# Kernel tuning notes

Measured on AMD Instinct MI355X. Metric: run time of the kernel, lower is better.

Reference implementation:

```python
import jax, jax.numpy as jnp
import numpy as np

H = 1024
EPS = 1e-5
N_ENT = 1000
TOP_K = 5


def _ln(x, g, b):
    mu = jnp.mean(x, axis=-1, keepdims=True)
    var = jnp.mean((x - mu) ** 2, axis=-1, keepdims=True)
    return (x - mu) * jax.lax.rsqrt(var + EPS) * g + b


def _gelu(x):
    return jax.nn.gelu(x, approximate=False)  # torch nn.GELU default (erf)


def setup_inputs() -> dict:
    key = jax.random.key(0)
    ks = jax.random.split(key, 24)
    s = 0.02
    inp = {
        'hidden_states': jax.random.normal(ks[0], (8, 2048, H), jnp.float32),
        'entity_embeddings': jax.random.normal(ks[1], (N_ENT, H), jnp.float32) * 0.01,
        # entity_encoder: H -> 2H -> H -> LN
        'ee_w1': jax.random.normal(ks[2], (H, 2 * H), jnp.float32) * s,
        'ee_b1': jnp.zeros((2 * H,), jnp.float32),
        'ee_w2': jax.random.normal(ks[3], (2 * H, H), jnp.float32) * s,
        'ee_b2': jnp.zeros((H,), jnp.float32),
        'ee_g': jnp.ones((H,), jnp.float32),
        'ee_beta': jnp.zeros((H,), jnp.float32),
        # relation_encoder: H -> H -> H -> LN
        're_w1': jax.random.normal(ks[4], (H, H), jnp.float32) * s,
        're_b1': jnp.zeros((H,), jnp.float32),
        're_w2': jax.random.normal(ks[5], (H, H), jnp.float32) * s,
        're_b2': jnp.zeros((H,), jnp.float32),
        're_g': jnp.ones((H,), jnp.float32),
        're_beta': jnp.zeros((H,), jnp.float32),
        # reasoning_network: 3H -> 2H -> H -> LN
        'rn_w1': jax.random.normal(ks[6], (3 * H, 2 * H), jnp.float32) * s,
        'rn_b1': jnp.zeros((2 * H,), jnp.float32),
        'rn_w2': jax.random.normal(ks[7], (2 * H, H), jnp.float32) * s,
        'rn_b2': jnp.zeros((H,), jnp.float32),
        'rn_g': jnp.ones((H,), jnp.float32),
        'rn_beta': jnp.zeros((H,), jnp.float32),
        # validation_network: H -> H/2 -> 1 -> sigmoid
        'vn_w1': jax.random.normal(ks[8], (H, H // 2), jnp.float32) * s,
        'vn_b1': jnp.zeros((H // 2,), jnp.float32),
        'vn_w2': jax.random.normal(ks[9], (H // 2, 1), jnp.float32) * s,
        'vn_b2': jnp.zeros((1,), jnp.float32),
    }
    return inp


def reference(hidden_states, entity_embeddings,
              ee_w1, ee_b1, ee_w2, ee_b2, ee_g, ee_beta,
              re_w1, re_b1, re_w2, re_b2, re_g, re_beta,
              rn_w1, rn_b1, rn_w2, rn_b2, rn_g, rn_beta,
              vn_w1, vn_b1, vn_w2, vn_b2):
    # entity encoder over all tokens: [B,S,H]
    entity_features = _ln(_gelu(hidden_states @ ee_w1 + ee_b1) @ ee_w2 + ee_b2, ee_g, ee_beta)

    # query=None path: relation encoder on mean-pooled hidden states [B,H]
    pooled = jnp.mean(hidden_states, axis=1)
    relation_features = _ln(_gelu(pooled @ re_w1 + re_b1) @ re_w2 + re_b2, re_g, re_beta)
    query_features = relation_features

    # similarity + top-k entity retrieval
    entity_similarities = query_features @ entity_embeddings.T  # [B, N_ENT]
    top_values, top_indices = jax.lax.top_k(entity_similarities, TOP_K)
    retrieved_entities = entity_embeddings[top_indices]  # [B, K, H]

    # reasoning input: [mean retrieved entity | relation | mean context]
    entity_vec = jnp.mean(retrieved_entities, axis=1)  # [B,H]
    context_vec = jnp.mean(hidden_states, axis=1)      # [B,H]
    reasoning_in = jnp.concatenate([entity_vec, relation_features, context_vec], axis=-1)  # [B,3H]
    reasoning_output = _ln(_gelu(reasoning_in @ rn_w1 + rn_b1) @ rn_w2 + rn_b2, rn_g, rn_beta)

    validation_scores = jax.nn.sigmoid(_gelu(reasoning_output @ vn_w1 + vn_b1) @ vn_w2 + vn_b2)

    return (entity_features, relation_features, retrieved_entities,
            entity_similarities, top_indices, reasoning_output, validation_scores)
```

## Files before the change

kernel.cpp:

```cpp
#include <hip/hip_runtime.h>
#include <math.h>

#define H 1024
#define SEQ 2048
#define BATCH 8
#define N_ENT 1000
#define TOPK 5
#define LN_EPS 1e-5f

using bf16x8 = __attribute__((ext_vector_type(8))) __bf16;
using f32x4  = __attribute__((ext_vector_type(4))) float;
#define AS1 __attribute__((address_space(1)))
#define AS3 __attribute__((address_space(3)))


__device__ __forceinline__ float gelu_fast(float x) {
    float z = fabsf(x) * 0.70710678118654752440f;
    float t = __builtin_amdgcn_rcpf(fmaf(0.3275911f, z, 1.0f));
    float p = fmaf(fmaf(fmaf(fmaf(1.061405429f, t, -1.453152027f), t, 1.421413741f),
                        t, -0.284496736f), t, 0.254829592f) * t;
    float e = __builtin_amdgcn_exp2f(-z * z * 1.44269504088896f);
    float erfz = fmaf(-p, e, 1.0f);
    float s = copysignf(erfz, x);
    return 0.5f * x * (1.0f + s);
}

__device__ __forceinline__ float sigmoidf_(float x) {
    return 1.0f / (1.0f + expf(-x));
}

__device__ __forceinline__ unsigned short f2bf(float f) {
    unsigned int u = __float_as_uint(f);
    unsigned int r = (u + 0x7fffu + ((u >> 16) & 1u)) >> 16;
    return (unsigned short)r;
}

__device__ float block_sum(float v, float* red) {
    for (int off = 32; off > 0; off >>= 1) v += __shfl_down(v, off, 64);
    int wid = threadIdx.x >> 6;
    int lane = threadIdx.x & 63;
    int nw = blockDim.x >> 6;
    if (lane == 0) red[wid] = v;
    __syncthreads();
    if (threadIdx.x == 0) {
        float s = 0.f;
        for (int i = 0; i < nw; ++i) s += red[i];
        red[0] = s;
    }
    __syncthreads();
    float r = red[0];
    __syncthreads();
    return r;
}


__global__ void f2bf_kernel(const float* __restrict__ in, unsigned short* __restrict__ out, int n) {
    int i = (blockIdx.x * blockDim.x + threadIdx.x) * 4;
    if (i >= n) return;
    float4 v = *(const float4*)(in + i);
    ushort4 o;
    o.x = f2bf(v.x); o.y = f2bf(v.y); o.z = f2bf(v.z); o.w = f2bf(v.w);
    *(ushort4*)(out + i) = o;
}

__global__ void transpose_bf_kernel(const float* __restrict__ in, unsigned short* __restrict__ out,
                                    int R, int C) {
    __shared__ float tile[32][33];
    int c0 = blockIdx.x * 32, r0 = blockIdx.y * 32;
    int tx = threadIdx.x & 31, ty = threadIdx.x >> 5;
#pragma unroll
    for (int i = 0; i < 32; i += 8)
        tile[ty + i][tx] = in[(size_t)(r0 + ty + i) * C + c0 + tx];
    __syncthreads();
#pragma unroll
    for (int i = 0; i < 32; i += 8)
        out[(size_t)(c0 + ty + i) * R + r0 + tx] = f2bf(tile[tx][ty + i]);
}


__global__ void pool1_kernel(const float* __restrict__ hs, float* __restrict__ part,
                             unsigned short* __restrict__ hsb) {
    int sc = blockIdx.x, b = blockIdx.y, t = threadIdx.x;
    size_t rowbase = (size_t)b * SEQ + sc * 64;
    const float* p = hs + rowbase * H + t * 4;
    float4 a = {0.f, 0.f, 0.f, 0.f};
    for (int s = 0; s < 64; ++s) {
        float4 v = *(const float4*)(p + (size_t)s * H);
        a.x += v.x; a.y += v.y; a.z += v.z; a.w += v.w;
        if (hsb) {
            ushort4 o;
            o.x = f2bf(v.x); o.y = f2bf(v.y); o.z = f2bf(v.z); o.w = f2bf(v.w);
            *(ushort4*)(hsb + (rowbase + s) * H + t * 4) = o;
        }
    }
    *(float4*)(part + ((size_t)b * 32 + sc) * H + t * 4) = a;
}

__global__ void pool2_kernel(const float* __restrict__ part, float* __restrict__ pooled) {
    int b = blockIdx.x, t = threadIdx.x;
    float4 s = {0.f, 0.f, 0.f, 0.f};
    for (int sc = 0; sc < 32; ++sc) {
        float4 v = *(const float4*)(part + ((size_t)b * 32 + sc) * H + t * 4);
        s.x += v.x; s.y += v.y; s.z += v.z; s.w += v.w;
    }
    float4 o = {s.x * (1.0f / SEQ), s.y * (1.0f / SEQ), s.z * (1.0f / SEQ), s.w * (1.0f / SEQ)};
    *(float4*)(pooled + (size_t)b * H + t * 4) = o;
}


template <int KRANGE>
__global__ void mlp_partial_kernel(const float* __restrict__ X, int ldx,
                                   const float* __restrict__ W, int N,
                                   float* __restrict__ part) {
    __shared__ float xs[8][KRANGE];
    int jb = blockIdx.x, ks = blockIdx.y, t = threadIdx.x;
    int k0 = ks * KRANGE;
    for (int i = t; i < 8 * KRANGE; i += 256) {
        int b = i / KRANGE, k = i % KRANGE;
        xs[b][k] = X[(size_t)b * ldx + k0 + k];
    }
    __syncthreads();
    int j = jb * 256 + t;
    float acc[8] = {};
    for (int k = 0; k < KRANGE; ++k) {
        float w = W[(size_t)(k0 + k) * N + j];
#pragma unroll
        for (int b = 0; b < 8; ++b) acc[b] = fmaf(xs[b][k], w, acc[b]);
    }
#pragma unroll
    for (int b = 0; b < 8; ++b) part[((size_t)ks * 8 + b) * N + j] = acc[b];
}

__global__ void mlp_reduce_gelu_kernel(const float* __restrict__ part, const float* __restrict__ bias,
                                       float* __restrict__ out, int N, int nks) {
    int b = blockIdx.y;
    int j = blockIdx.x * 256 + threadIdx.x;
    float s = bias[j];
    for (int ks = 0; ks < nks; ++ks) s += part[((size_t)ks * 8 + b) * N + j];
    out[(size_t)b * N + j] = gelu_fast(s);
}

__global__ void mlp_reduce_ln_kernel(const float* __restrict__ part, const float* __restrict__ bias,
                                     const float* __restrict__ g, const float* __restrict__ be,
                                     float* __restrict__ out, int nks) {
    __shared__ float red[32];
    int b = blockIdx.x, t = threadIdx.x;
    float s = bias[t];
    for (int ks = 0; ks < nks; ++ks) s += part[((size_t)ks * 8 + b) * H + t];
    float mu = block_sum(s, red) * (1.0f / H);
    float d = s - mu;
    float var = block_sum(d * d, red) * (1.0f / H);
    out[(size_t)b * H + t] = d * rsqrtf(var + LN_EPS) * g[t] + be[t];
}


__global__ void sim_kernel(const float* __restrict__ rel, const float* __restrict__ ent,
                           float* __restrict__ sims) {
    __shared__ float rl[8 * H];
    int t = threadIdx.x;
    for (int i = t; i < 8 * H; i += 256) rl[i] = rel[i];
    __syncthreads();
    int e = blockIdx.x * 4 + (t >> 6);
    int lane = t & 63;
    float ev[16];
    const float* ep = ent + (size_t)e * H;
#pragma unroll
    for (int i = 0; i < 16; ++i) ev[i] = ep[lane + i * 64];
#pragma unroll
    for (int b = 0; b < 8; ++b) {
        float a = 0.f;
#pragma unroll
        for (int i = 0; i < 16; ++i) a = fmaf(ev[i], rl[b * H + lane + i * 64], a);
        for (int off = 32; off > 0; off >>= 1) a += __shfl_down(a, off, 64);
        if (lane == 0) sims[b * N_ENT + e] = a;
    }
}

__global__ void topk_kernel(const float* __restrict__ sims, float* __restrict__ out_idx_f,
                            int* __restrict__ idx_i) {
    __shared__ float v[1024];
    __shared__ float rv[4];
    __shared__ int ri[4];
    int b = blockIdx.x, t = threadIdx.x;
    for (int i = t; i < 1024; i += 256) v[i] = (i < N_ENT) ? sims[b * N_ENT + i] : -INFINITY;
    __syncthreads();
    for (int k = 0; k < TOPK; ++k) {
        float best = -INFINITY;
        int bi = 0x7fffffff;
        for (int i = t; i < 1024; i += 256) {
            float x = v[i];
            if (x > best || (x == best && i < bi)) { best = x; bi = i; }
        }
        for (int off = 32; off > 0; off >>= 1) {
            float ov = __shfl_down(best, off, 64);
            int oi = __shfl_down(bi, off, 64);
            if (ov > best || (ov == best && oi < bi)) { best = ov; bi = oi; }
        }
        if ((t & 63) == 0) { rv[t >> 6] = best; ri[t >> 6] = bi; }
        __syncthreads();
        if (t == 0) {
            for (int w = 1; w < 4; ++w)
                if (rv[w] > rv[0] || (rv[w] == rv[0] && ri[w] < ri[0])) { rv[0] = rv[w]; ri[0] = ri[w]; }
            int sel = ri[0];
            out_idx_f[b * TOPK + k] = (float)sel;
            idx_i[b * TOPK + k] = sel;
            v[sel] = -INFINITY;
        }
        __syncthreads();
    }
}

__global__ void gather_concat_kernel(const float* __restrict__ ent, const int* __restrict__ idx,
                                     const float* __restrict__ rel, const float* __restrict__ pooled,
                                     float* __restrict__ retrieved, float* __restrict__ xin) {
    int b = blockIdx.x, h = threadIdx.x;
    float acc = 0.f;
    for (int k = 0; k < TOPK; ++k) {
        float v = ent[(size_t)idx[b * TOPK + k] * H + h];
        retrieved[((size_t)b * TOPK + k) * H + h] = v;
        acc += v;
    }
    float* xb = xin + (size_t)b * 3 * H;
    xb[h] = acc * (1.0f / TOPK);
    xb[H + h] = rel[b * H + h];
    xb[2 * H + h] = pooled[b * H + h];
}

__global__ void vn_final_kernel(const float* __restrict__ part, const float* __restrict__ b1,
                                const float* __restrict__ w2, const float* __restrict__ b2,
                                float* __restrict__ vs, int nks) {
    __shared__ float red[32];
    int b = blockIdx.x, t = threadIdx.x;
    float s = b1[t];
    for (int ks = 0; ks < nks; ++ks) s += part[((size_t)ks * 8 + b) * 512 + t];
    float c = gelu_fast(s) * w2[t];
    float tot = block_sum(c, red);
    if (t == 0) vs[b] = sigmoidf_(tot + b2[0]);
}

template <int GELU_BF16_OUT>
__global__ __launch_bounds__(512, 2) void gemm256_8ph(const unsigned short* __restrict__ A,
                                                      const unsigned short* __restrict__ Bt,
                                                      const float* __restrict__ bias,
                                                      void* __restrict__ Cout,
                                                      int M, int N, int K) {
    __shared__ __align__(16) unsigned short As[4][128 * 64];
    __shared__ __align__(16) unsigned short Bs[4][128 * 64];
    const int tid = threadIdx.x;
    const int lane = tid & 63;
    const int w = tid >> 6;
    const int wm2 = w >> 2;
    const int wn4 = w & 3;

    const int Np = N >> 8;
    const int nwg = gridDim.x;
    int bid = blockIdx.x;
    int s = bid;
    if ((nwg & 7) == 0) s = (bid & 7) * (nwg >> 3) + (bid >> 3);
    const int m0 = (s / Np) << 8;
    const int n0 = (s % Np) << 8;

    const int nT = K >> 6;

    const int l7 = lane & 7;
    const int lrow0 = w * 16 + (lane >> 3);
    const int lrow1 = lrow0 + 8;
    const int kel0 = ((l7 ^ (lrow0 & 7)) << 3);
    const int kel1 = ((l7 ^ (lrow1 & 7)) << 3);
    const unsigned short* pa0 = A + (size_t)(m0 + lrow0) * K + kel0;
    const unsigned short* pa1 = A + (size_t)(m0 + lrow1) * K + kel1;
    const unsigned short* pb0 = Bt + (size_t)(n0 + lrow0) * K + kel0;
    const unsigned short* pb1 = Bt + (size_t)(n0 + lrow1) * K + kel1;
    const size_t halfstep = (size_t)128 * K;
    const int dst0 = (w * 16) * 64;
    const int dst1 = dst0 + 8 * 64;

    auto stageA = [&](int t, int half) {
        if (t >= nT) return;
        int slot = (2 * t + half) & 3;
        int koff = t << 6;
        __builtin_amdgcn_global_load_lds((AS1 void*)(pa0 + half * halfstep + koff),
                                         (AS3 void*)(&As[slot][dst0]), 16, 0, 0);
        __builtin_amdgcn_global_load_lds((AS1 void*)(pa1 + half * halfstep + koff),
                                         (AS3 void*)(&As[slot][dst1]), 16, 0, 0);
    };
    auto stageB = [&](int t, int half) {
        if (t >= nT) return;
        int slot = (2 * t + half) & 3;
        int koff = t << 6;
        __builtin_amdgcn_global_load_lds((AS1 void*)(pb0 + half * halfstep + koff),
                                         (AS3 void*)(&Bs[slot][dst0]), 16, 0, 0);
        __builtin_amdgcn_global_load_lds((AS1 void*)(pb1 + half * halfstep + koff),
                                         (AS3 void*)(&Bs[slot][dst1]), 16, 0, 0);
    };

    const int arow = lane & 15;
    const int xk0 = (((lane >> 4) << 4)) ^ (l7 << 4);
    const int xk1 = (64 + ((lane >> 4) << 4)) ^ (l7 << 4);
    auto ldf = [&](const unsigned short* slotbase, int rowbase, int xk) -> bf16x8 {
        return *(const bf16x8*)((const char*)slotbase + (rowbase + arow) * 128 + xk);
    };

    f32x4 acc[8][4] = {};

    stageA(0, 0); stageA(0, 1); stageB(0, 0); stageB(0, 1);
    asm volatile("s_waitcnt vmcnt(4)" ::: "memory");
    stageA(1, 0); stageB(1, 0); stageB(1, 1);
    asm volatile("s_waitcnt vmcnt(6)" ::: "memory");
    __builtin_amdgcn_s_barrier();

    bf16x8 af0[4][2], af1[4][2], bf0[2][2], bf1[2][2];

    for (int T = 0; T < nT; ++T) {
        const unsigned short* Aslot0 = As[(2 * T) & 3];
        const unsigned short* Aslot1 = As[(2 * T + 1) & 3];
        const unsigned short* Bslot0 = Bs[(2 * T) & 3];
        const unsigned short* Bslot1 = Bs[(2 * T + 1) & 3];

#pragma unroll
        for (int ii = 0; ii < 4; ++ii) {
            af0[ii][0] = ldf(Aslot0, ii * 32 + wm2 * 16, xk0);
            af0[ii][1] = ldf(Aslot0, ii * 32 + wm2 * 16, xk1);
        }
#pragma unroll
        for (int jj = 0; jj < 2; ++jj) {
            bf0[jj][0] = ldf(Bslot0, jj * 64 + wn4 * 16, xk0);
            bf0[jj][1] = ldf(Bslot0, jj * 64 + wn4 * 16, xk1);
        }
        stageA(T + 1, 1);
        __builtin_amdgcn_s_barrier();
        __builtin_amdgcn_s_setprio(1);
#pragma unroll
        for (int ii = 0; ii < 4; ++ii)
#pragma unroll
            for (int jj = 0; jj < 2; ++jj) {
                acc[ii][jj] = __builtin_amdgcn_mfma_f32_16x16x32_bf16(af0[ii][0], bf0[jj][0], acc[ii][jj], 0, 0, 0);
                acc[ii][jj] = __builtin_amdgcn_mfma_f32_16x16x32_bf16(af0[ii][1], bf0[jj][1], acc[ii][jj], 0, 0, 0);
            }
        __builtin_amdgcn_s_setprio(0);
        __builtin_amdgcn_s_barrier();

#pragma unroll
        for (int jj = 0; jj < 2; ++jj) {
            bf1[jj][0] = ldf(Bslot1, jj * 64 + wn4 * 16, xk0);
            bf1[jj][1] = ldf(Bslot1, jj * 64 + wn4 * 16, xk1);
        }
        stageA(T + 2, 0);
        __builtin_amdgcn_s_barrier();
        __builtin_amdgcn_s_setprio(1);
#pragma unroll
        for (int ii = 0; ii < 4; ++ii)
#pragma unroll
            for (int jj = 0; jj < 2; ++jj) {
                acc[ii][2 + jj] = __builtin_amdgcn_mfma_f32_16x16x32_bf16(af0[ii][0], bf1[jj][0], acc[ii][2 + jj], 0, 0, 0);
                acc[ii][2 + jj] = __builtin_amdgcn_mfma_f32_16x16x32_bf16(af0[ii][1], bf1[jj][1], acc[ii][2 + jj], 0, 0, 0);
            }
        __builtin_amdgcn_s_setprio(0);
        __builtin_amdgcn_s_barrier();

#pragma unroll
        for (int ii = 0; ii < 4; ++ii) {
            af1[ii][0] = ldf(Aslot1, ii * 32 + wm2 * 16, xk0);
            af1[ii][1] = ldf(Aslot1, ii * 32 + wm2 * 16, xk1);
        }
        stageB(T + 2, 0);
        __builtin_amdgcn_s_barrier();
        __builtin_amdgcn_s_setprio(1);
#pragma unroll
        for (int ii = 0; ii < 4; ++ii)
#pragma unroll
            for (int jj = 0; jj < 2; ++jj) {
                acc[4 + ii][jj] = __builtin_amdgcn_mfma_f32_16x16x32_bf16(af1[ii][0], bf0[jj][0], acc[4 + ii][jj], 0, 0, 0);
                acc[4 + ii][jj] = __builtin_amdgcn_mfma_f32_16x16x32_bf16(af1[ii][1], bf0[jj][1], acc[4 + ii][jj], 0, 0, 0);
            }
        __builtin_amdgcn_s_setprio(0);
        __builtin_amdgcn_s_barrier();

        stageB(T + 2, 1);
        if (T + 3 <= nT) {
            asm volatile("s_waitcnt vmcnt(6)" ::: "memory");
        } else {
            asm volatile("s_waitcnt vmcnt(0)" ::: "memory");
        }
        __builtin_amdgcn_s_barrier();
        __builtin_amdgcn_s_setprio(1);
#pragma unroll
        for (int ii = 0; ii < 4; ++ii)
#pragma unroll
            for (int jj = 0; jj < 2; ++jj) {
                acc[4 + ii][2 + jj] = __builtin_amdgcn_mfma_f32_16x16x32_bf16(af1[ii][0], bf1[jj][0], acc[4 + ii][2 + jj], 0, 0, 0);
                acc[4 + ii][2 + jj] = __builtin_amdgcn_mfma_f32_16x16x32_bf16(af1[ii][1], bf1[jj][1], acc[4 + ii][2 + jj], 0, 0, 0);
            }
        __builtin_amdgcn_s_setprio(0);
        __builtin_amdgcn_s_barrier();
    }

    const int cn = lane & 15;
    const int rbase = (lane >> 4) * 4;
#pragma unroll
    for (int i = 0; i < 8; ++i) {
        int mbase = m0 + (i >> 2) * 128 + (i & 3) * 32 + wm2 * 16 + rbase;
#pragma unroll
        for (int j = 0; j < 4; ++j) {
            int n = n0 + (j >> 1) * 128 + (j & 1) * 64 + wn4 * 16 + cn;
            float bv = bias[n];
#pragma unroll
            for (int r = 0; r < 4; ++r) {
                float c = acc[i][j][r] + bv;
                if (GELU_BF16_OUT) {
                    c = gelu_fast(c);
                    ((unsigned short*)Cout)[(size_t)(mbase + r) * N + n] = f2bf(c);
                } else {
                    ((float*)Cout)[(size_t)(mbase + r) * N + n] = c;
                }
            }
        }
    }
}

__global__ void ln_rows_kernel(float* __restrict__ x, const float* __restrict__ g,
                               const float* __restrict__ beta) {
    __shared__ float red[32];
    float* p = x + (size_t)blockIdx.x * H;
    int t = threadIdx.x;
    float4 v = *(const float4*)(p + t * 4);
    float s = v.x + v.y + v.z + v.w;
    float mu = block_sum(s, red) * (1.0f / H);
    float4 d = { v.x - mu, v.y - mu, v.z - mu, v.w - mu };
    float d2 = d.x * d.x + d.y * d.y + d.z * d.z + d.w * d.w;
    float var = block_sum(d2, red) * (1.0f / H);
    float inv = rsqrtf(var + LN_EPS);
    float4 gg = *(const float4*)(g + t * 4);
    float4 bb = *(const float4*)(beta + t * 4);
    float4 o = { d.x * inv * gg.x + bb.x, d.y * inv * gg.y + bb.y,
                 d.z * inv * gg.z + bb.z, d.w * inv * gg.w + bb.w };
    *(float4*)(p + t * 4) = o;
}


extern "C" void kernel_launch(void* const* d_in, const int* in_sizes, int n_in,
                              void* d_out, int out_size, void* d_ws, size_t ws_size,
                              hipStream_t stream) {
    const float* hs     = (const float*)d_in[0];
    const float* ent    = (const float*)d_in[1];
    const float* ee_w1  = (const float*)d_in[2];
    const float* ee_b1  = (const float*)d_in[3];
    const float* ee_w2  = (const float*)d_in[4];
    const float* ee_b2  = (const float*)d_in[5];
    const float* ee_g   = (const float*)d_in[6];
    const float* ee_be  = (const float*)d_in[7];
    const float* re_w1  = (const float*)d_in[8];
    const float* re_b1  = (const float*)d_in[9];
    const float* re_w2  = (const float*)d_in[10];
    const float* re_b2  = (const float*)d_in[11];
    const float* re_g   = (const float*)d_in[12];
    const float* re_be  = (const float*)d_in[13];
    const float* rn_w1  = (const float*)d_in[14];
    const float* rn_b1  = (const float*)d_in[15];
    const float* rn_w2  = (const float*)d_in[16];
    const float* rn_b2  = (const float*)d_in[17];
    const float* rn_g   = (const float*)d_in[18];
    const float* rn_be  = (const float*)d_in[19];
    const float* vn_w1  = (const float*)d_in[20];
    const float* vn_b1  = (const float*)d_in[21];
    const float* vn_w2  = (const float*)d_in[22];
    const float* vn_b2  = (const float*)d_in[23];

    float* out = (float*)d_out;
    float* ef   = out;
    float* rel  = ef + (size_t)BATCH * SEQ * H;
    float* retr = rel + BATCH * H;
    float* sims = retr + BATCH * TOPK * H;
    float* tidx = sims + BATCH * N_ENT;
    float* ro   = tidx + BATCH * TOPK;
    float* vs   = ro + BATCH * H;

    float* ws = (float*)d_ws;
    size_t o = 0;
    float* pooled = ws + o; o += 8192;
    int*   idx_i  = (int*)(ws + o); o += 64;
    float* xin    = ws + o; o += 8 * 3 * H;
    float* h1r    = ws + o; o += 8 * H;
    float* h1n    = ws + o; o += 8 * 2 * H;
    float* part   = ws + o; o += 24 * 8 * 2048;
    unsigned short* w1t = (unsigned short*)(ws + o); o += (2048 * 1024) / 2;
    unsigned short* w2t = (unsigned short*)(ws + o); o += (2048 * 1024) / 2;
    unsigned short* hsb = (unsigned short*)(ws + o);

    long long avail = (long long)(ws_size / 4) - (long long)o;
    int chunk = (int)(avail / 1536);
    chunk &= ~255;
    int total = BATCH * SEQ;
    if (chunk > total) chunk = total;
    if (chunk < 256) chunk = 256;
    bool full = (chunk >= total);
    unsigned short* midb = hsb + (size_t)chunk * H;

    transpose_bf_kernel<<<dim3(2048 / 32, 1024 / 32), 256, 0, stream>>>(ee_w1, w1t, 1024, 2048);
    transpose_bf_kernel<<<dim3(1024 / 32, 2048 / 32), 256, 0, stream>>>(ee_w2, w2t, 2048, 1024);

    pool1_kernel<<<dim3(32, BATCH), 256, 0, stream>>>(hs, part, full ? hsb : nullptr);
    pool2_kernel<<<BATCH, 256, 0, stream>>>(part, pooled);

    mlp_partial_kernel<64><<<dim3(4, 16), 256, 0, stream>>>(pooled, H, re_w1, H, part);
    mlp_reduce_gelu_kernel<<<dim3(4, 8), 256, 0, stream>>>(part, re_b1, h1r, H, 16);
    mlp_partial_kernel<64><<<dim3(4, 16), 256, 0, stream>>>(h1r, H, re_w2, H, part);
    mlp_reduce_ln_kernel<<<BATCH, 1024, 0, stream>>>(part, re_b2, re_g, re_be, rel, 16);

    sim_kernel<<<250, 256, 0, stream>>>(rel, ent, sims);
    topk_kernel<<<BATCH, 256, 0, stream>>>(sims, tidx, idx_i);
    gather_concat_kernel<<<BATCH, 1024, 0, stream>>>(ent, idx_i, rel, pooled, retr, xin);

    mlp_partial_kernel<128><<<dim3(8, 24), 256, 0, stream>>>(xin, 3 * H, rn_w1, 2 * H, part);
    mlp_reduce_gelu_kernel<<<dim3(8, 8), 256, 0, stream>>>(part, rn_b1, h1n, 2 * H, 24);
    mlp_partial_kernel<128><<<dim3(4, 16), 256, 0, stream>>>(h1n, 2 * H, rn_w2, H, part);
    mlp_reduce_ln_kernel<<<BATCH, 1024, 0, stream>>>(part, rn_b2, rn_g, rn_be, ro, 16);

    mlp_partial_kernel<128><<<dim3(2, 8), 256, 0, stream>>>(ro, H, vn_w1, 512, part);
    vn_final_kernel<<<BATCH, 512, 0, stream>>>(part, vn_b1, vn_w2, vn_b2, vs, 8);

    for (int r0 = 0; r0 < total; r0 += chunk) {
        int m = total - r0;
        if (m > chunk) m = chunk;
        if (!full) {
            int nconv = m * H;
            f2bf_kernel<<<(nconv / 4 + 255) / 256, 256, 0, stream>>>(hs + (size_t)r0 * H, hsb, nconv);
        }
        unsigned short* a1 = full ? (hsb + (size_t)r0 * H) : hsb;
        gemm256_8ph<1><<<(m / 256) * (2048 / 256), 512, 0, stream>>>(a1, w1t, ee_b1, midb,
                                                                     m, 2048, 1024);
        gemm256_8ph<0><<<(m / 256) * (1024 / 256), 512, 0, stream>>>(midb, w2t, ee_b2,
                                                                     ef + (size_t)r0 * H,
                                                                     m, 1024, 2048);
    }
    ln_rows_kernel<<<total, 256, 0, stream>>>(ef, ee_g, ee_be);
}
```

Before: 537.1 us.

## Fuse small-path kernels into one persistent kernel with grid barriers

Replaces the chain of about fourteen small launches (pool reduce, relation MLP, similarity, top-k, gather, reasoning MLP, validation) with a single 64-block persistent kernel that uses an atomic global barrier between stages. The two weight transposes are also merged into one launch. The goal is to cut per-launch overhead and idle gaps on the small serial path. The cost is that 64 blocks give little parallelism for the weight-streaming MLP stages, and the spin barrier relies on all 64 blocks being co-resident.

```diff
diff --git a/kernel.cpp b/kernel.cpp
--- a/kernel.cpp
+++ b/kernel.cpp
@@ -7,6 +7,7 @@
 #define N_ENT 1000
 #define TOPK 5
 #define LN_EPS 1e-5f
+#define NB_SMALL 64
 
 using bf16x8 = __attribute__((ext_vector_type(8))) __bf16;
 using f32x4  = __attribute__((ext_vector_type(4))) float;
@@ -53,6 +54,24 @@
     return r;
 }
 
+__device__ __forceinline__ void gbar(unsigned* cnt, unsigned* gen) {
+    __syncthreads();
+    if (threadIdx.x == 0) {
+        __threadfence();
+        unsigned g = __hip_atomic_load(gen, __ATOMIC_RELAXED, __HIP_MEMORY_SCOPE_AGENT);
+        unsigned a = __hip_atomic_fetch_add(cnt, 1u, __ATOMIC_ACQ_REL, __HIP_MEMORY_SCOPE_AGENT);
+        if (a == NB_SMALL - 1) {
+            __hip_atomic_store(cnt, 0u, __ATOMIC_RELAXED, __HIP_MEMORY_SCOPE_AGENT);
+            __hip_atomic_fetch_add(gen, 1u, __ATOMIC_ACQ_REL, __HIP_MEMORY_SCOPE_AGENT);
+        } else {
+            while (__hip_atomic_load(gen, __ATOMIC_ACQUIRE, __HIP_MEMORY_SCOPE_AGENT) == g)
+                __builtin_amdgcn_s_sleep(1);
+        }
+        __threadfence();
+    }
+    __syncthreads();
+}
+
 
 __global__ void f2bf_kernel(const float* __restrict__ in, unsigned short* __restrict__ out, int n) {
     int i = (blockIdx.x * blockDim.x + threadIdx.x) * 4;
@@ -63,10 +82,14 @@
     *(ushort4*)(out + i) = o;
 }
 
-__global__ void transpose_bf_kernel(const float* __restrict__ in, unsigned short* __restrict__ out,
-                                    int R, int C) {
+__global__ void transpose_both_kernel(const float* __restrict__ w1, unsigned short* __restrict__ o1,
+                                      const float* __restrict__ w2, unsigned short* __restrict__ o2) {
     __shared__ float tile[32][33];
-    int c0 = blockIdx.x * 32, r0 = blockIdx.y * 32;
+    int bid = blockIdx.x;
+    const float* in; unsigned short* out; int R, C, bx, by;
+    if (bid < 2048) { in = w1; out = o1; R = 1024; C = 2048; bx = bid & 63; by = bid >> 6; }
+    else { bid -= 2048; in = w2; out = o2; R = 2048; C = 1024; bx = bid & 31; by = bid >> 5; }
+    int c0 = bx * 32, r0 = by * 32;
     int tx = threadIdx.x & 31, ty = threadIdx.x >> 5;
 #pragma unroll
     for (int i = 0; i < 32; i += 8)
@@ -96,146 +119,211 @@
     *(float4*)(part + ((size_t)b * 32 + sc) * H + t * 4) = a;
 }
 
-__global__ void pool2_kernel(const float* __restrict__ part, float* __restrict__ pooled) {
-    int b = blockIdx.x, t = threadIdx.x;
-    float4 s = {0.f, 0.f, 0.f, 0.f};
-    for (int sc = 0; sc < 32; ++sc) {
-        float4 v = *(const float4*)(part + ((size_t)b * 32 + sc) * H + t * 4);
-        s.x += v.x; s.y += v.y; s.z += v.z; s.w += v.w;
-    }
-    float4 o = {s.x * (1.0f / SEQ), s.y * (1.0f / SEQ), s.z * (1.0f / SEQ), s.w * (1.0f / SEQ)};
-    *(float4*)(pooled + (size_t)b * H + t * 4) = o;
-}
-
-
-template <int KRANGE>
-__global__ void mlp_partial_kernel(const float* __restrict__ X, int ldx,
-                                   const float* __restrict__ W, int N,
-                                   float* __restrict__ part) {
-    __shared__ float xs[8][KRANGE];
-    int jb = blockIdx.x, ks = blockIdx.y, t = threadIdx.x;
-    int k0 = ks * KRANGE;
-    for (int i = t; i < 8 * KRANGE; i += 256) {
-        int b = i / KRANGE, k = i % KRANGE;
-        xs[b][k] = X[(size_t)b * ldx + k0 + k];
+
+__device__ void mlp_partial_dev(const float* X, int ldx, const float* W, int N,
+                                float* part, int jb, int ks, int KR, float* xs) {
+    int t = threadIdx.x;
+    int k0 = ks * KR;
+    __syncthreads();
+    for (int i = t; i < 8 * KR; i += 256) {
+        int b = i / KR, k = i - b * KR;
+        xs[b * KR + k] = X[(size_t)b * ldx + k0 + k];
     }
     __syncthreads();
     int j = jb * 256 + t;
     float acc[8] = {};
-    for (int k = 0; k < KRANGE; ++k) {
+    for (int k = 0; k < KR; ++k) {
         float w = W[(size_t)(k0 + k) * N + j];
 #pragma unroll
-        for (int b = 0; b < 8; ++b) acc[b] = fmaf(xs[b][k], w, acc[b]);
-    }
-#pragma unroll
-    for (int b = 0; b < 8; ++b) part[((size_t)ks * 8 + b) * N + j] = acc[b];
-}
-
-__global__ void mlp_reduce_gelu_kernel(const float* __restrict__ part, const float* __restrict__ bias,
-                                       float* __restrict__ out, int N, int nks) {
-    int b = blockIdx.y;
-    int j = blockIdx.x * 256 + threadIdx.x;
-    float s = bias[j];
-    for (int ks = 0; ks < nks; ++ks) s += part[((size_t)ks * 8 + b) * N + j];
-    out[(size_t)b * N + j] = gelu_fast(s);
-}
-
-__global__ void mlp_reduce_ln_kernel(const float* __restrict__ part, const float* __restrict__ bias,
-                                     const float* __restrict__ g, const float* __restrict__ be,
-                                     float* __restrict__ out, int nks) {
-    __shared__ float red[32];
-    int b = blockIdx.x, t = threadIdx.x;
-    float s = bias[t];
-    for (int ks = 0; ks < nks; ++ks) s += part[((size_t)ks * 8 + b) * H + t];
-    float mu = block_sum(s, red) * (1.0f / H);
-    float d = s - mu;
-    float var = block_sum(d * d, red) * (1.0f / H);
-    out[(size_t)b * H + t] = d * rsqrtf(var + LN_EPS) * g[t] + be[t];
-}
-
-
-__global__ void sim_kernel(const float* __restrict__ rel, const float* __restrict__ ent,
-                           float* __restrict__ sims) {
-    __shared__ float rl[8 * H];
+        for (int b = 0; b < 8; ++b) acc[b] = fmaf(xs[b * KR + k], w, acc[b]);
+    }
+#pragma unroll
+    for (int b = 0; b < 8; ++b) part[((size_t)(ks * 8 + b)) * N + j] = acc[b];
+}
+
+__device__ void reduce_ln_256(const float* part, const float* bias, const float* g,
+                              const float* be, float* out, int nks, int b, float* red) {
     int t = threadIdx.x;
-    for (int i = t; i < 8 * H; i += 256) rl[i] = rel[i];
-    __syncthreads();
-    int e = blockIdx.x * 4 + (t >> 6);
-    int lane = t & 63;
-    float ev[16];
-    const float* ep = ent + (size_t)e * H;
-#pragma unroll
-    for (int i = 0; i < 16; ++i) ev[i] = ep[lane + i * 64];
-#pragma unroll
-    for (int b = 0; b < 8; ++b) {
-        float a = 0.f;
-#pragma unroll
-        for (int i = 0; i < 16; ++i) a = fmaf(ev[i], rl[b * H + lane + i * 64], a);
-        for (int off = 32; off > 0; off >>= 1) a += __shfl_down(a, off, 64);
-        if (lane == 0) sims[b * N_ENT + e] = a;
-    }
-}
-
-__global__ void topk_kernel(const float* __restrict__ sims, float* __restrict__ out_idx_f,
-                            int* __restrict__ idx_i) {
-    __shared__ float v[1024];
-    __shared__ float rv[4];
-    __shared__ int ri[4];
-    int b = blockIdx.x, t = threadIdx.x;
-    for (int i = t; i < 1024; i += 256) v[i] = (i < N_ENT) ? sims[b * N_ENT + i] : -INFINITY;
-    __syncthreads();
-    for (int k = 0; k < TOPK; ++k) {
-        float best = -INFINITY;
-        int bi = 0x7fffffff;
-        for (int i = t; i < 1024; i += 256) {
-            float x = v[i];
-            if (x > best || (x == best && i < bi)) { best = x; bi = i; }
-        }
-        for (int off = 32; off > 0; off >>= 1) {
-            float ov = __shfl_down(best, off, 64);
-            int oi = __shfl_down(bi, off, 64);
-            if (ov > best || (ov == best && oi < bi)) { best = ov; bi = oi; }
-        }
-        if ((t & 63) == 0) { rv[t >> 6] = best; ri[t >> 6] = bi; }
+    float4 s = *(const float4*)(bias + t * 4);
+    for (int ks = 0; ks < nks; ++ks) {
+        float4 p = *(const float4*)(part + (((size_t)(ks * 8 + b)) << 10) + t * 4);
+        s.x += p.x; s.y += p.y; s.z += p.z; s.w += p.w;
+    }
+    float mu = block_sum(s.x + s.y + s.z + s.w, red) * (1.0f / H);
+    float4 d = {s.x - mu, s.y - mu, s.z - mu, s.w - mu};
+    float var = block_sum(d.x * d.x + d.y * d.y + d.z * d.z + d.w * d.w, red) * (1.0f / H);
+    float inv = rsqrtf(var + LN_EPS);
+    float4 gg = *(const float4*)(g + t * 4);
+    float4 bb = *(const float4*)(be + t * 4);
+    float4 o = {d.x * inv * gg.x + bb.x, d.y * inv * gg.y + bb.y,
+                d.z * inv * gg.z + bb.z, d.w * inv * gg.w + bb.w};
+    *(float4*)(out + ((size_t)b << 10) + t * 4) = o;
+}
+
+__global__ __launch_bounds__(256) void small_path_kernel(
+    float* part,
+    float* pooled, float* h1r, float* h1n, float* xin, int* idx_i,
+    const float* __restrict__ ent,
+    const float* re_w1, const float* re_b1, const float* re_w2, const float* re_b2,
+    const float* re_g, const float* re_be,
+    const float* rn_w1, const float* rn_b1, const float* rn_w2, const float* rn_b2,
+    const float* rn_g, const float* rn_be,
+    const float* vn_w1, const float* vn_b1, const float* vn_w2, const float* vn_b2,
+    float* rel, float* sims, float* tidx, float* retr, float* ro, float* vs,
+    unsigned* bar) {
+    __shared__ __align__(16) unsigned char smraw[33 * 1024];
+    float* xs  = (float*)smraw;
+    float* rl  = (float*)smraw;
+    float* tkv = (float*)smraw;
+    float* trv = (float*)(smraw + 4096);
+    int*   tri = (int*)(smraw + 4112);
+    float* red = (float*)smraw;
+
+    unsigned* cnt = bar;
+    unsigned* gen = bar + 1;
+    const int bid = blockIdx.x;
+    const int t = threadIdx.x;
+
+    {
+        int gid = bid * 256 + t;
+        if (gid < 8 * H) {
+            int b = gid >> 10, h = gid & 1023;
+            float s = 0.f;
+            for (int sc = 0; sc < 32; ++sc) s += part[(((size_t)(b * 32 + sc)) << 10) + h];
+            pooled[((size_t)b << 10) + h] = s * (1.0f / SEQ);
+        }
+    }
+    gbar(cnt, gen);
+
+    mlp_partial_dev(pooled, H, re_w1, H, part, bid & 3, bid >> 2, 64, xs);
+    gbar(cnt, gen);
+
+    if (bid < 32) {
+        int jb = bid & 3, b = bid >> 2;
+        int j = jb * 256 + t;
+        float s = re_b1[j];
+        for (int ks = 0; ks < 16; ++ks) s += part[((size_t)(ks * 8 + b)) * H + j];
+        h1r[((size_t)b << 10) + j] = gelu_fast(s);
+    }
+    gbar(cnt, gen);
+
+    mlp_partial_dev(h1r, H, re_w2, H, part, bid & 3, bid >> 2, 64, xs);
+    gbar(cnt, gen);
+
+    if (bid < 8) reduce_ln_256(part, re_b2, re_g, re_be, rel, 16, bid, red);
+    gbar(cnt, gen);
+
+    {
+        for (int i = t; i < 8 * H; i += 256) rl[i] = rel[i];
         __syncthreads();
-        if (t == 0) {
-            for (int w = 1; w < 4; ++w)
-                if (rv[w] > rv[0] || (rv[w] == rv[0] && ri[w] < ri[0])) { rv[0] = rv[w]; ri[0] = ri[w]; }
-            int sel = ri[0];
-            out_idx_f[b * TOPK + k] = (float)sel;
-            idx_i[b * TOPK + k] = sel;
-            v[sel] = -INFINITY;
-        }
+        int widx = t >> 6, lane = t & 63;
+        for (int r = 0; r < 4; ++r) {
+            int e = bid * 16 + r * 4 + widx;
+            if (e < N_ENT) {
+                const float* ep = ent + (size_t)e * H;
+                float ev[16];
+#pragma unroll
+                for (int i = 0; i < 16; ++i) ev[i] = ep[lane + i * 64];
+#pragma unroll
+                for (int b = 0; b < 8; ++b) {
+                    float a = 0.f;
+#pragma unroll
+                    for (int i = 0; i < 16; ++i) a = fmaf(ev[i], rl[b * H + lane + i * 64], a);
+                    for (int off = 32; off > 0; off >>= 1) a += __shfl_down(a, off, 64);
+                    if (lane == 0) sims[b * N_ENT + e] = a;
+                }
+            }
+        }
+    }
+    gbar(cnt, gen);
+
+    if (bid < 8) {
+        int b = bid;
+        for (int i = t; i < 1024; i += 256) tkv[i] = (i < N_ENT) ? sims[b * N_ENT + i] : -INFINITY;
         __syncthreads();
-    }
-}
-
-__global__ void gather_concat_kernel(const float* __restrict__ ent, const int* __restrict__ idx,
-                                     const float* __restrict__ rel, const float* __restrict__ pooled,
-                                     float* __restrict__ retrieved, float* __restrict__ xin) {
-    int b = blockIdx.x, h = threadIdx.x;
-    float acc = 0.f;
-    for (int k = 0; k < TOPK; ++k) {
-        float v = ent[(size_t)idx[b * TOPK + k] * H + h];
-        retrieved[((size_t)b * TOPK + k) * H + h] = v;
-        acc += v;
-    }
-    float* xb = xin + (size_t)b * 3 * H;
-    xb[h] = acc * (1.0f / TOPK);
-    xb[H + h] = rel[b * H + h];
-    xb[2 * H + h] = pooled[b * H + h];
-}
-
-__global__ void vn_final_kernel(const float* __restrict__ part, const float* __restrict__ b1,
-                                const float* __restrict__ w2, const float* __restrict__ b2,
-                                float* __restrict__ vs, int nks) {
-    __shared__ float red[32];
-    int b = blockIdx.x, t = threadIdx.x;
-    float s = b1[t];
-    for (int ks = 0; ks < nks; ++ks) s += part[((size_t)ks * 8 + b) * 512 + t];
-    float c = gelu_fast(s) * w2[t];
-    float tot = block_sum(c, red);
-    if (t == 0) vs[b] = sigmoidf_(tot + b2[0]);
+        for (int k = 0; k < TOPK; ++k) {
+            float best = -INFINITY;
+            int bi = 0x7fffffff;
+            for (int i = t; i < 1024; i += 256) {
+                float x = tkv[i];
+                if (x > best || (x == best && i < bi)) { best = x; bi = i; }
+            }
+            for (int off = 32; off > 0; off >>= 1) {
+                float ov = __shfl_down(best, off, 64);
+                int oi = __shfl_down(bi, off, 64);
+                if (ov > best || (ov == best && oi < bi)) { best = ov; bi = oi; }
+            }
+            if ((t & 63) == 0) { trv[t >> 6] = best; tri[t >> 6] = bi; }
+            __syncthreads();
+            if (t == 0) {
+                for (int w = 1; w < 4; ++w)
+                    if (trv[w] > trv[0] || (trv[w] == trv[0] && tri[w] < tri[0])) { trv[0] = trv[w]; tri[0] = tri[w]; }
+                int sel = tri[0];
+                tidx[b * TOPK + k] = (float)sel;
+                idx_i[b * TOPK + k] = sel;
+                tkv[sel] = -INFINITY;
+            }
+            __syncthreads();
+        }
+    }
+    gbar(cnt, gen);
+
+    if (bid < 8) {
+        int b = bid;
+#pragma unroll
+        for (int u = 0; u < 4; ++u) {
+            int h = u * 256 + t;
+            float acc = 0.f;
+            for (int k = 0; k < TOPK; ++k) {
+                float v = ent[(size_t)idx_i[b * TOPK + k] * H + h];
+                retr[((size_t)(b * TOPK + k)) * H + h] = v;
+                acc += v;
+            }
+            xin[(size_t)b * 3 * H + h] = acc * (1.0f / TOPK);
+            xin[(size_t)b * 3 * H + H + h] = rel[b * H + h];
+            xin[(size_t)b * 3 * H + 2 * H + h] = pooled[b * H + h];
+        }
+    }
+    gbar(cnt, gen);
+
+    for (int r = 0; r < 3; ++r) {
+        int u = bid + 64 * r;
+        mlp_partial_dev(xin, 3 * H, rn_w1, 2 * H, part, u & 7, u >> 3, 128, xs);
+    }
+    gbar(cnt, gen);
+
+    {
+        int jb = bid & 7, b = bid >> 3;
+        int j = jb * 256 + t;
+        float s = rn_b1[j];
+        for (int ks = 0; ks < 24; ++ks) s += part[((size_t)(ks * 8 + b)) * 2048 + j];
+        h1n[(size_t)b * 2048 + j] = gelu_fast(s);
+    }
+    gbar(cnt, gen);
+
+    mlp_partial_dev(h1n, 2 * H, rn_w2, H, part, bid & 3, bid >> 2, 128, xs);
+    gbar(cnt, gen);
+
+    if (bid < 8) reduce_ln_256(part, rn_b2, rn_g, rn_be, ro, 16, bid, red);
+    gbar(cnt, gen);
+
+    if (bid < 16) mlp_partial_dev(ro, H, vn_w1, 512, part, bid & 1, bid >> 1, 128, xs);
+    else { __syncthreads(); __syncthreads(); }
+    gbar(cnt, gen);
+
+    if (bid < 8) {
+        int b = bid;
+        float c = 0.f;
+#pragma unroll
+        for (int u = 0; u < 2; ++u) {
+            int e = u * 256 + t;
+            float s = vn_b1[e];
+            for (int ks = 0; ks < 8; ++ks) s += part[((size_t)(ks * 8 + b)) * 512 + e];
+            c += gelu_fast(s) * vn_w2[e];
+        }
+        float tot = block_sum(c, red);
+        if (t == 0) vs[b] = sigmoidf_(tot + vn_b2[0]);
+    }
 }
 
 template <int GELU_BF16_OUT>
@@ -479,6 +567,7 @@
     size_t o = 0;
     float* pooled = ws + o; o += 8192;
     int*   idx_i  = (int*)(ws + o); o += 64;
+    unsigned* bar = (unsigned*)(ws + o); o += 16;
     float* xin    = ws + o; o += 8 * 3 * H;
     float* h1r    = ws + o; o += 8 * H;
     float* h1n    = ws + o; o += 8 * 2 * H;
@@ -496,28 +585,18 @@
     bool full = (chunk >= total);
     unsigned short* midb = hsb + (size_t)chunk * H;
 
-    transpose_bf_kernel<<<dim3(2048 / 32, 1024 / 32), 256, 0, stream>>>(ee_w1, w1t, 1024, 2048);
-    transpose_bf_kernel<<<dim3(1024 / 32, 2048 / 32), 256, 0, stream>>>(ee_w2, w2t, 2048, 1024);
+    hipMemsetAsync(bar, 0, 2 * sizeof(unsigned), stream);
 
     pool1_kernel<<<dim3(32, BATCH), 256, 0, stream>>>(hs, part, full ? hsb : nullptr);
-    pool2_kernel<<<BATCH, 256, 0, stream>>>(part, pooled);
-
-    mlp_partial_kernel<64><<<dim3(4, 16), 256, 0, stream>>>(pooled, H, re_w1, H, part);
-    mlp_reduce_gelu_kernel<<<dim3(4, 8), 256, 0, stream>>>(part, re_b1, h1r, H, 16);
-    mlp_partial_kernel<64><<<dim3(4, 16), 256, 0, stream>>>(h1r, H, re_w2, H, part);
-    mlp_reduce_ln_kernel<<<BATCH, 1024, 0, stream>>>(part, re_b2, re_g, re_be, rel, 16);
-
-    sim_kernel<<<250, 256, 0, stream>>>(rel, ent, sims);
-    topk_kernel<<<BATCH, 256, 0, stream>>>(sims, tidx, idx_i);
-    gather_concat_kernel<<<BATCH, 1024, 0, stream>>>(ent, idx_i, rel, pooled, retr, xin);
-
-    mlp_partial_kernel<128><<<dim3(8, 24), 256, 0, stream>>>(xin, 3 * H, rn_w1, 2 * H, part);
-    mlp_reduce_gelu_kernel<<<dim3(8, 8), 256, 0, stream>>>(part, rn_b1, h1n, 2 * H, 24);
-    mlp_partial_kernel<128><<<dim3(4, 16), 256, 0, stream>>>(h1n, 2 * H, rn_w2, H, part);
-    mlp_reduce_ln_kernel<<<BATCH, 1024, 0, stream>>>(part, rn_b2, rn_g, rn_be, ro, 16);
-
-    mlp_partial_kernel<128><<<dim3(2, 8), 256, 0, stream>>>(ro, H, vn_w1, 512, part);
-    vn_final_kernel<<<BATCH, 512, 0, stream>>>(part, vn_b1, vn_w2, vn_b2, vs, 8);
+
+    transpose_both_kernel<<<4096, 256, 0, stream>>>(ee_w1, w1t, ee_w2, w2t);
+
+    small_path_kernel<<<NB_SMALL, 256, 0, stream>>>(
+        part, pooled, h1r, h1n, xin, idx_i, ent,
+        re_w1, re_b1, re_w2, re_b2, re_g, re_be,
+        rn_w1, rn_b1, rn_w2, rn_b2, rn_g, rn_be,
+        vn_w1, vn_b1, vn_w2, vn_b2,
+        rel, sims, tidx, retr, ro, vs, bar);
 
     for (int r0 = 0; r0 < total; r0 += chunk) {
         int m = total - r0;
```

After: 662.2 us. +23.3%, slower.
